# Kernel tuning notes

Hardware: AMD Instinct MI355X
Metric: run time of the kernel (lower is better)

## Reference

```python
import jax, jax.numpy as jnp
import numpy as np
from jax import lax

NUM_CHANNELS = 32
PROT_SECTION = 4
PROT_SIZE = NUM_CHANNELS * PROT_SECTION  # 128
BATCH = 128
SEQ_LEN = 8194


def setup_inputs() -> dict:
    key = jax.random.key(0)
    ks = jax.random.split(key, 6)
    input_seq = jax.random.randint(ks[0], (BATCH, SEQ_LEN), 0, 26)
    emb = jax.random.normal(ks[1], (26, 5), dtype=jnp.float32)
    conv_w = jax.random.normal(ks[2], (NUM_CHANNELS, 5, 3), dtype=jnp.float32) * 0.1
    conv_b = jnp.zeros((NUM_CHANNELS,), dtype=jnp.float32)
    W_a = jax.random.normal(ks[3], (PROT_SIZE, PROT_SIZE), dtype=jnp.float32) / np.sqrt(PROT_SIZE)
    v_a = jax.random.normal(ks[4], (PROT_SIZE,), dtype=jnp.float32)
    return {"input_seq": input_seq, "emb": emb, "conv_w": conv_w,
            "conv_b": conv_b, "W_a": W_a, "v_a": v_a}


def reference(input_seq, emb, conv_w, conv_b, W_a, v_a):
    # Embedding lookup: [B, L, 5] -> [B, 5, L]
    x = emb[input_seq].transpose(0, 2, 1)
    # Conv1d(5 -> C, k=3, valid) + bias + ReLU  (dropout is identity in eval)
    y = lax.conv_general_dilated(x, conv_w, window_strides=(1,), padding='VALID',
                                 dimension_numbers=('NCH', 'OIH', 'NCH'))
    y = jax.nn.relu(y + conv_b[None, :, None])  # [B, C, L-2]
    B, C, PL = y.shape
    S = PROT_SECTION
    new_L = PL // S
    rem = PL % S
    head = rem // 2
    tail = PL - (rem - head)
    y = y[:, :, head:tail].reshape(B, C * S, new_L)  # [B, D, N], D = C*S
    # Batched self-attention pooling (original loops over batch in Python)
    # energies[b, n] = v_a @ tanh(W_a @ H_b)
    e = jnp.einsum('d,bdn->bn', v_a, jnp.tanh(jnp.einsum('de,ben->bdn', W_a, y)))
    w = jax.nn.softmax(e, axis=-1)  # stable softmax; same math as unstable F.softmax
    ctx = jnp.einsum('bn,bdn->bd', w, y)  # [B, D]
    return ctx
```

## Files before the change

kernel.cpp:

```cpp
#include <hip/hip_runtime.h>

#define LSEQ 8194

typedef _Float16 f16x8 __attribute__((ext_vector_type(8)));
typedef _Float16 f16x2 __attribute__((ext_vector_type(2)));
typedef __attribute__((ext_vector_type(4))) float f32x4;

static __device__ __forceinline__ float tanh_fast(float x){
    float p = __expf(2.0f * x);
    float r = __builtin_amdgcn_rcpf(1.0f + p);
    return 1.0f - 2.0f * r;
}
static __device__ __forceinline__ unsigned h3relu(unsigned a, unsigned b, unsigned c){
    union { f16x2 h; unsigned u; } x, y, z, r;
    x.u = a; y.u = b; z.u = c;
    f16x2 s = x.h + y.h + z.h;
    f16x2 zero = { (_Float16)0.0f, (_Float16)0.0f };
    r.h = __builtin_elementwise_max(s, zero);
    return r.u;
}
static __device__ __forceinline__ unsigned hpack(float a, float b){
    union { f16x2 h; unsigned u; } pk;
    pk.h = (f16x2){ (_Float16)a, (_Float16)b };
    return pk.u;
}
#define ROR_ADD(x, ctrl) ({ \
    union { float f; int i; } _s, _r; _s.f = (x); \
    _r.i = __builtin_amdgcn_update_dpp(0, _s.i, (ctrl), 0xF, 0xF, true); \
    (x) + _r.f; })

__global__ __launch_bounds__(256) void k_setup(
        const float* __restrict__ emb, const float* __restrict__ cw,
        const float* __restrict__ cb, const float* __restrict__ Wa,
        unsigned* __restrict__ tblG, unsigned* __restrict__ wahG)
{
    int gid = blockIdx.x*256 + threadIdx.x;
    if (gid < 1248){
        int k = gid / 416;
        int rem = gid - k*416;
        int l = rem >> 4;
        int cp = rem & 15;
        int c0 = cp*2;
        float v0 = 0.f, v1 = 0.f;
        #pragma unroll
        for (int i = 0; i < 5; i++){
            float e = emb[l*5 + i];
            v0 += cw[(c0*5 + i)*3 + k] * e;
            v1 += cw[((c0+1)*5 + i)*3 + k] * e;
        }
        if (k == 2){ v0 += cb[c0]; v1 += cb[c0+1]; }
        tblG[k*520 + l*20 + (cp & 3)*4 + (cp >> 2)] = hpack(v0, v1);
    }
    for (int i = gid; i < 8192; i += 1280){
        float2 t = ((const float2*)Wa)[i];
        unsigned byteoff = ((unsigned)i << 2) ^ ((((unsigned)i >> 6) & 7u) << 4);
        *(unsigned*)((char*)wahG + byteoff) = hpack(t.x, t.y);
    }
}

__global__ __launch_bounds__(256, 2) void k_fused(
        const int* __restrict__ seq, const unsigned* __restrict__ tblG,
        const unsigned* __restrict__ wahG, const float* __restrict__ va,
        float* __restrict__ part, float* __restrict__ stats)
{
    __shared__ __align__(16) unsigned wahL[8192];
    __shared__ __align__(16) unsigned tblH[1560];
    __shared__ unsigned short seqw16[4][132];
    __shared__ __align__(16) float vaL[128];

    int tid = threadIdx.x;
    int b   = blockIdx.y;
    int x   = blockIdx.x;
    int n0  = x * 128;

    #pragma unroll
    for (int j = 0; j < 8; j++)
        ((uint4*)wahL)[tid + j*256] = ((const uint4*)wahG)[tid + j*256];
    for (int i = tid; i < 390; i += 256)
        ((uint4*)tblH)[i] = ((const uint4*)tblG)[i];
    if (tid < 128) vaL[tid] = va[tid];
    const int* sb = seq + (size_t)b * LSEQ;
    for (int i = tid; i < 4*132; i += 256){
        int s = i / 132, off = i - s*132;
        if (off < 130)
            seqw16[s][off] = (unsigned short)(sb[s*2048 + n0 + off] * 80);
    }
    __syncthreads();

    int w = tid >> 6, lane = tid & 63;
    int m = lane & 15, q = lane >> 4;
    const char* tb0 = (const char*)tblH + q*16;
    const char* tb1 = tb0 + 2080;
    const char* tb2 = tb1 + 2080;

    uint4 vfr0[4], vfr1[4];
    {
        int base = w*32 + m;
        unsigned V[4][4];
        #pragma unroll
        for (int s = 0; s < 4; s++){
            unsigned oa = seqw16[s][base];
            unsigned ob = seqw16[s][base+1];
            unsigned oc = seqw16[s][base+2];
            uint4 t0 = *(const uint4*)(tb0 + oa);
            uint4 t1 = *(const uint4*)(tb1 + ob);
            uint4 t2 = *(const uint4*)(tb2 + oc);
            V[s][0] = h3relu(t0.x, t1.x, t2.x);
            V[s][1] = h3relu(t0.y, t1.y, t2.y);
            V[s][2] = h3relu(t0.z, t1.z, t2.z);
            V[s][3] = h3relu(t0.w, t1.w, t2.w);
        }
        #pragma unroll
        for (int ki = 0; ki < 4; ki++){
            uint4 o;
            o.x = __builtin_amdgcn_perm(V[1][ki], V[0][ki], 0x05040100u);
            o.y = __builtin_amdgcn_perm(V[3][ki], V[2][ki], 0x05040100u);
            o.z = __builtin_amdgcn_perm(V[1][ki], V[0][ki], 0x07060302u);
            o.w = __builtin_amdgcn_perm(V[3][ki], V[2][ki], 0x07060302u);
            vfr0[ki] = o;
        }
    }
    {
        int base = w*32 + 16 + m;
        unsigned V[4][4];
        #pragma unroll
        for (int s = 0; s < 4; s++){
            unsigned oa = seqw16[s][base];
            unsigned ob = seqw16[s][base+1];
            unsigned oc = seqw16[s][base+2];
            uint4 t0 = *(const uint4*)(tb0 + oa);
            uint4 t1 = *(const uint4*)(tb1 + ob);
            uint4 t2 = *(const uint4*)(tb2 + oc);
            V[s][0] = h3relu(t0.x, t1.x, t2.x);
            V[s][1] = h3relu(t0.y, t1.y, t2.y);
            V[s][2] = h3relu(t0.z, t1.z, t2.z);
            V[s][3] = h3relu(t0.w, t1.w, t2.w);
        }
        #pragma unroll
        for (int ki = 0; ki < 4; ki++){
            uint4 o;
            o.x = __builtin_amdgcn_perm(V[1][ki], V[0][ki], 0x05040100u);
            o.y = __builtin_amdgcn_perm(V[3][ki], V[2][ki], 0x05040100u);
            o.z = __builtin_amdgcn_perm(V[1][ki], V[0][ki], 0x07060302u);
            o.w = __builtin_amdgcn_perm(V[3][ki], V[2][ki], 0x07060302u);
            vfr1[ki] = o;
        }
    }

    float ep0 = 0.f, ep1 = 0.f;
    #pragma unroll
    for (int h = 0; h < 2; h++){
        f32x4 acc0[4], acc1[4];
        #pragma unroll
        for (int dd = 0; dd < 4; dd++){
            acc0[dd] = (f32x4){0.f, 0.f, 0.f, 0.f};
            acc1[dd] = (f32x4){0.f, 0.f, 0.f, 0.f};
        }
        #pragma unroll
        for (int ki = 0; ki < 4; ki++){
            uint4 af[4];
            #pragma unroll
            for (int dd = 0; dd < 4; dd++){
                int dt = h*4 + dd;
                unsigned abyte = (unsigned)((dt*16 + m)*256 + ki*64 + q*16)
                               ^ (((unsigned)(m & 7)) << 4);
                af[dd] = *(const uint4*)((const char*)wahL + abyte);
            }
            union { uint4 u; f16x8 f; } b0, b1;
            b0.u = vfr0[ki]; b1.u = vfr1[ki];
            #pragma unroll
            for (int dd = 0; dd < 4; dd++){
                union { uint4 u; f16x8 f; } a; a.u = af[dd];
                acc0[dd] = __builtin_amdgcn_mfma_f32_16x16x32_f16(a.f, b0.f, acc0[dd], 0, 0, 0);
                acc1[dd] = __builtin_amdgcn_mfma_f32_16x16x32_f16(a.f, b1.f, acc1[dd], 0, 0, 0);
            }
        }
        #pragma unroll
        for (int dd = 0; dd < 4; dd++){
            int dt = h*4 + dd;
            const f32x4 vg = *(const f32x4*)&vaL[dt*16 + q*4];
            ep0 += vg[0] * tanh_fast(acc0[dd][0]);
            ep0 += vg[1] * tanh_fast(acc0[dd][1]);
            ep0 += vg[2] * tanh_fast(acc0[dd][2]);
            ep0 += vg[3] * tanh_fast(acc0[dd][3]);
            ep1 += vg[0] * tanh_fast(acc1[dd][0]);
            ep1 += vg[1] * tanh_fast(acc1[dd][1]);
            ep1 += vg[2] * tanh_fast(acc1[dd][2]);
            ep1 += vg[3] * tanh_fast(acc1[dd][3]);
        }
    }
    ep0 += __shfl_xor(ep0, 16);
    ep0 += __shfl_xor(ep0, 32);
    ep1 += __shfl_xor(ep1, 16);
    ep1 += __shfl_xor(ep1, 32);

    float w0 = __expf(ep0);
    float w1 = __expf(ep1);
    float Sw = w0 + w1;

    float accp[32];
    #pragma unroll
    for (int ki = 0; ki < 4; ki++){
        union { uint4 u; f16x2 h[4]; } v0, v1;
        v0.u = vfr0[ki]; v1.u = vfr1[ki];
        #pragma unroll
        for (int t = 0; t < 4; t++){
            accp[ki*8 + ((t>>1)<<2) + (t&1)*1 + 0] = 0.f;
        }
        accp[ki*8 + 0] = w0 * (float)v0.h[0][0] + w1 * (float)v1.h[0][0];
        accp[ki*8 + 1] = w0 * (float)v0.h[0][1] + w1 * (float)v1.h[0][1];
        accp[ki*8 + 2] = w0 * (float)v0.h[1][0] + w1 * (float)v1.h[1][0];
        accp[ki*8 + 3] = w0 * (float)v0.h[1][1] + w1 * (float)v1.h[1][1];
        accp[ki*8 + 4] = w0 * (float)v0.h[2][0] + w1 * (float)v1.h[2][0];
        accp[ki*8 + 5] = w0 * (float)v0.h[2][1] + w1 * (float)v1.h[2][1];
        accp[ki*8 + 6] = w0 * (float)v0.h[3][0] + w1 * (float)v1.h[3][0];
        accp[ki*8 + 7] = w0 * (float)v0.h[3][1] + w1 * (float)v1.h[3][1];
    }

    #pragma unroll
    for (int j = 0; j < 32; j++){
        accp[j] = ROR_ADD(accp[j], 0x121);
        accp[j] = ROR_ADD(accp[j], 0x122);
        accp[j] = ROR_ADD(accp[j], 0x124);
        accp[j] = ROR_ADD(accp[j], 0x128);
    }
    Sw = ROR_ADD(Sw, 0x121);
    Sw = ROR_ADD(Sw, 0x122);
    Sw = ROR_ADD(Sw, 0x124);
    Sw = ROR_ADD(Sw, 0x128);

    size_t chunk = ((size_t)b*16 + x)*4 + w;
    if (m == 0){
        float* pd = part + chunk*128;
        #pragma unroll
        for (int ki = 0; ki < 4; ki++){
            float4 lo = { accp[ki*8+0], accp[ki*8+1], accp[ki*8+2], accp[ki*8+3] };
            float4 hi = { accp[ki*8+4], accp[ki*8+5], accp[ki*8+6], accp[ki*8+7] };
            *(float4*)(pd + ki*32 + q*8)     = lo;
            *(float4*)(pd + ki*32 + q*8 + 4) = hi;
        }
    }
    if (lane == 0)
        stats[chunk] = Sw;
}

__global__ __launch_bounds__(128) void kb2_finish(const float* __restrict__ part,
        const float* __restrict__ stats, float* __restrict__ out)
{
    int b = blockIdx.x, d = threadIdx.x;
    const float* st = stats + (size_t)b*64;
    float S = 0.f;
    #pragma unroll 8
    for (int c = 0; c < 64; c++) S += st[c];
    const float* p = part + (size_t)b*64*128 + d;
    float s = 0.f;
    #pragma unroll 8
    for (int c = 0; c < 64; c++) s += p[c*128];
    out[b*128 + d] = s / S;
}

extern "C" void kernel_launch(void* const* d_in, const int* in_sizes, int n_in,
                              void* d_out, int out_size, void* d_ws, size_t ws_size,
                              hipStream_t stream)
{
    const int*   seq = (const int*)d_in[0];
    const float* emb = (const float*)d_in[1];
    const float* cw  = (const float*)d_in[2];
    const float* cb  = (const float*)d_in[3];
    const float* Wa  = (const float*)d_in[4];
    const float* va  = (const float*)d_in[5];
    float* out = (float*)d_out;

    char* wsb = (char*)d_ws;
    float*    part  = (float*)wsb;
    float*    stats = (float*)(wsb + (8<<20));
    unsigned* tblG  = (unsigned*)(wsb + (12<<20));
    unsigned* wahG  = (unsigned*)(wsb + (12<<20) + 32768);

    k_setup   <<<5,            256, 0, stream>>>(emb, cw, cb, Wa, tblG, wahG);
    k_fused   <<<dim3(16,128), 256, 0, stream>>>(seq, tblG, wahG, va, part, stats);
    kb2_finish<<<128,          128, 0, stream>>>(part, stats, out);
}
```

Before: 94.71 us.

## Pre-swizzle W_a into MFMA fragment order and read it straight from global

The prep kernel now writes W_a as fp16 in per-lane MFMA A-fragment order, so each lane's 16-byte fragment sits contiguously. The fused kernel drops its 32KB shared-memory copy of W_a and loads fragments directly from global (L2/L1-cached) into registers, eight at a time. This removes the per-block LDS fill and the shared reads, and may let more blocks fit per CU. In exchange, every wave issues global loads for the weights, which depend on cache hits for latency. It also removes dead zero-initialisation stores.

```diff
diff --git a/kernel.cpp b/kernel.cpp
--- a/kernel.cpp
+++ b/kernel.cpp
@@ -51,10 +51,18 @@
         if (k == 2){ v0 += cb[c0]; v1 += cb[c0+1]; }
         tblG[k*520 + l*20 + (cp & 3)*4 + (cp >> 2)] = hpack(v0, v1);
     }
-    for (int i = gid; i < 8192; i += 1280){
-        float2 t = ((const float2*)Wa)[i];
-        unsigned byteoff = ((unsigned)i << 2) ^ ((((unsigned)i >> 6) & 7u) << 4);
-        *(unsigned*)((char*)wahG + byteoff) = hpack(t.x, t.y);
+    for (int u = gid; u < 2048; u += 1280){
+        int lane = u & 63, dtki = u >> 6;
+        int dt = dtki >> 2, ki = dtki & 3;
+        int m = lane & 15, q = lane >> 4;
+        const float2* src = (const float2*)Wa + ((dt*16 + m)*64 + ki*16 + q*4);
+        float2 s0 = src[0], s1 = src[1], s2 = src[2], s3 = src[3];
+        uint4 o;
+        o.x = hpack(s0.x, s0.y);
+        o.y = hpack(s1.x, s1.y);
+        o.z = hpack(s2.x, s2.y);
+        o.w = hpack(s3.x, s3.y);
+        ((uint4*)wahG)[u] = o;
     }
 }
 
@@ -63,7 +71,6 @@
         const unsigned* __restrict__ wahG, const float* __restrict__ va,
         float* __restrict__ part, float* __restrict__ stats)
 {
-    __shared__ __align__(16) unsigned wahL[8192];
     __shared__ __align__(16) unsigned tblH[1560];
     __shared__ unsigned short seqw16[4][132];
     __shared__ __align__(16) float vaL[128];
@@ -73,9 +80,6 @@
     int x   = blockIdx.x;
     int n0  = x * 128;
 
-    #pragma unroll
-    for (int j = 0; j < 8; j++)
-        ((uint4*)wahL)[tid + j*256] = ((const uint4*)wahG)[tid + j*256];
     for (int i = tid; i < 390; i += 256)
         ((uint4*)tblH)[i] = ((const uint4*)tblG)[i];
     if (tid < 128) vaL[tid] = va[tid];
@@ -92,6 +96,7 @@
     const char* tb0 = (const char*)tblH + q*16;
     const char* tb1 = tb0 + 2080;
     const char* tb2 = tb1 + 2080;
+    const uint4* wa4 = (const uint4*)wahG + lane;
 
     uint4 vfr0[4], vfr1[4];
     {
@@ -157,22 +162,26 @@
             acc1[dd] = (f32x4){0.f, 0.f, 0.f, 0.f};
         }
         #pragma unroll
-        for (int ki = 0; ki < 4; ki++){
-            uint4 af[4];
+        for (int kp = 0; kp < 2; kp++){
+            uint4 af[8];
             #pragma unroll
-            for (int dd = 0; dd < 4; dd++){
-                int dt = h*4 + dd;
-                unsigned abyte = (unsigned)((dt*16 + m)*256 + ki*64 + q*16)
-                               ^ (((unsigned)(m & 7)) << 4);
-                af[dd] = *(const uint4*)((const char*)wahL + abyte);
-            }
-            union { uint4 u; f16x8 f; } b0, b1;
-            b0.u = vfr0[ki]; b1.u = vfr1[ki];
+            for (int kk = 0; kk < 2; kk++)
+                #pragma unroll
+                for (int dd = 0; dd < 4; dd++){
+                    int dt = h*4 + dd, ki = kp*2 + kk;
+                    af[kk*4+dd] = wa4[(dt*4 + ki) << 6];
+                }
             #pragma unroll
-            for (int dd = 0; dd < 4; dd++){
-                union { uint4 u; f16x8 f; } a; a.u = af[dd];
-                acc0[dd] = __builtin_amdgcn_mfma_f32_16x16x32_f16(a.f, b0.f, acc0[dd], 0, 0, 0);
-                acc1[dd] = __builtin_amdgcn_mfma_f32_16x16x32_f16(a.f, b1.f, acc1[dd], 0, 0, 0);
+            for (int kk = 0; kk < 2; kk++){
+                int ki = kp*2 + kk;
+                union { uint4 u; f16x8 f; } b0, b1;
+                b0.u = vfr0[ki]; b1.u = vfr1[ki];
+                #pragma unroll
+                for (int dd = 0; dd < 4; dd++){
+                    union { uint4 u; f16x8 f; } a; a.u = af[kk*4+dd];
+                    acc0[dd] = __builtin_amdgcn_mfma_f32_16x16x32_f16(a.f, b0.f, acc0[dd], 0, 0, 0);
+                    acc1[dd] = __builtin_amdgcn_mfma_f32_16x16x32_f16(a.f, b1.f, acc1[dd], 0, 0, 0);
+                }
             }
         }
         #pragma unroll
@@ -203,10 +212,6 @@
     for (int ki = 0; ki < 4; ki++){
         union { uint4 u; f16x2 h[4]; } v0, v1;
         v0.u = vfr0[ki]; v1.u = vfr1[ki];
-        #pragma unroll
-        for (int t = 0; t < 4; t++){
-            accp[ki*8 + ((t>>1)<<2) + (t&1)*1 + 0] = 0.f;
-        }
         accp[ki*8 + 0] = w0 * (float)v0.h[0][0] + w1 * (float)v1.h[0][0];
         accp[ki*8 + 1] = w0 * (float)v0.h[0][1] + w1 * (float)v1.h[0][1];
         accp[ki*8 + 2] = w0 * (float)v0.h[1][0] + w1 * (float)v1.h[1][0];
```

Result: no change. 93.96 us (median of 3 runs) (-0.8%).
